# Kernel tuning notes

Hardware: AMD Instinct MI355X
Metric: run time of the kernel (lower is better)

## Reference

```python
import jax, jax.numpy as jnp
import numpy as np

V = 17  # number of skeleton joints (hard-coded in the torch module)
NUM_SUBSET = 3

def _dam_mask():
    # Reproduces the Python masking loops: zero block [12:17,12:17] and rows/cols {3,6,7,9,10}
    m = np.ones((V, V), np.float32)
    m[12:17, 12:17] = 0.0
    for j in (3, 6, 7, 9, 10):
        m[j, :] = 0.0
        m[:, j] = 0.0
    return jnp.asarray(m)

def setup_inputs() -> dict:
    key = jax.random.key(0)
    ks = jax.random.split(key, 8)
    N, Cin, Cout, T, G = 64, 64, 64, 256, 8
    return {
        "x": jax.random.normal(ks[0], (N, Cin, T, V), jnp.float32),
        "A_base": jax.random.uniform(ks[1], (NUM_SUBSET, V, V), jnp.float32),  # fixed adjacency buffer
        "DA": 0.01 * jax.random.normal(ks[2], (NUM_SUBSET, G, V, V), jnp.float32),   # DecoupleA param
        "DAM": 0.01 * jax.random.normal(ks[3], (NUM_SUBSET, G, V, V), jnp.float32),  # DecoupleAM param (masked, detached)
        "conv_w": jax.random.normal(ks[4], (NUM_SUBSET * Cout, Cin), jnp.float32) * (2.0 / Cin) ** 0.5,  # 1x1 conv
        "conv_b": jnp.zeros((NUM_SUBSET * Cout,), jnp.float32),
        "se_w": jax.random.normal(ks[5], (3,), jnp.float32) * 0.5,  # conv2_1: Conv1d(1,1,k=3,pad=1,no bias)
        "bn_gamma": jnp.full((Cout,), 1e-6, jnp.float32),  # bn_init(bn, 1e-6)
        "bn_beta": jnp.zeros((Cout,), jnp.float32),
    }

def reference(x, A_base, DA, DAM, conv_w, conv_b, se_w, bn_gamma, bn_beta):
    G = DA.shape[1]
    Cout = bn_gamma.shape[0]
    N, Cin, T, _ = x.shape
    # --- adjacency assembly: A (buffer, broadcast over groups) + DecoupleA + masked DecoupleAM ---
    A = A_base[:, None] + DA + DAM * _dam_mask()              # [3, G, V, V]
    # torch .repeat(1, out//groups, 1, 1) tiles along channel axis; + 0.04 from A_final loop
    A_final = jnp.tile(A, (1, Cout // G, 1, 1)) + 0.04        # [3, Cout, V, V]
    # --- 1x1 conv C_in -> 3*C_out ---
    m = jnp.einsum('nctv,kc->nktv', x, conv_w) + conv_b[None, :, None, None]
    m = m.reshape(N, NUM_SUBSET, Cout, T, V)
    # --- grouped adjacency aggregation (A_final has no batch dependence) ---
    m = jnp.einsum('nkctv,kcvw->nctw', m, A_final)            # [N, Cout, T, V]
    # --- SE-style channel attention: global avg pool -> Conv1d(k=3) over channels -> sigmoid gate ---
    p = m.mean(axis=(2, 3))                                   # [N, Cout]
    pp = jnp.pad(p, ((0, 0), (1, 1)))
    g = se_w[0] * pp[:, :-2] + se_w[1] * pp[:, 1:-1] + se_w[2] * pp[:, 2:]
    q = m + m * jax.nn.sigmoid(g)[:, :, None, None]
    # --- BatchNorm2d (training mode: batch stats over N,T,V) ---
    mu = q.mean(axis=(0, 2, 3), keepdims=True)
    var = q.var(axis=(0, 2, 3), keepdims=True)
    q = bn_gamma[None, :, None, None] * (q - mu) * jax.lax.rsqrt(var + 1e-5) + bn_beta[None, :, None, None]
    # --- residual (down == identity since in_channels == out_channels) and ReLU ---
    return jax.nn.relu(q + x)
```

## Files before the change

kernel.cpp:

```cpp
#include <hip/hip_runtime.h>
#include <math.h>

#define NN 64
#define CIN 64
#define COUT 64
#define TT 256
#define VV 17
#define NSUB 3
#define GG 8

#define WS_MB 0
#define WS_WBF 12288
#define WS_PSUM 18432
#define WS_SSQ 22528
#define WS_ACOEF 0
#define WS_BCOEF 4096
#define M2BF_BYTE_OFF 131072ull
#define M2BF_NEED (M2BF_BYTE_OFF + 2ull * 64 * 64 * 256 * 17)

typedef short bh8 __attribute__((ext_vector_type(8)));
typedef float f32x4 __attribute__((ext_vector_type(4)));
typedef float f32x16 __attribute__((ext_vector_type(16)));
typedef unsigned short u16t;

__device__ __forceinline__ unsigned bf16r(float f) {
    unsigned u = __builtin_bit_cast(unsigned, f);
    return (u + 0x7fffu + ((u >> 16) & 1u)) >> 16;
}
__device__ __forceinline__ float bf2f(unsigned us) {
    return __builtin_bit_cast(float, us << 16);
}

__device__ __forceinline__ float mfull(const float* Ab, const float* DA, const float* DAM,
                                       int s, int g, int v, int w) {
    const unsigned bad = (1u << 3) | (1u << 6) | (1u << 7) | (1u << 9) | (1u << 10);
    float mask = ((v >= 12 && w >= 12) || ((bad >> v) & 1) || ((bad >> w) & 1)) ? 0.f : 1.f;
    int src = ((s * GG + g) * VV + v) * VV + w;
    return Ab[(s * VV + v) * VV + w] + DA[src] + DAM[src] * mask + 0.04f;
}

__global__ void gcn_prep(const float* __restrict__ Ab, const float* __restrict__ DA,
                         const float* __restrict__ DAM, const float* __restrict__ convw,
                         float* __restrict__ ws) {
    int t0 = blockIdx.x * 256 + threadIdx.x;
    int stride = gridDim.x * 256;
    u16t* wbf = (u16t*)(ws + WS_WBF);
    for (int i = t0; i < 192 * 64; i += stride) wbf[i] = (u16t)bf16r(convw[i]);
    u16t* mb = (u16t*)(ws + WS_MB);
    for (int i = t0; i < NSUB * GG * 32 * 32; i += stride) {
        int k = i & 31, w = (i >> 5) & 31, g = (i >> 10) & 7, s = i >> 13;
        u16t val = 0;
        if (w < VV && k < VV) val = (u16t)bf16r(mfull(Ab, DA, DAM, s, g, k, w));
        mb[i] = val;
    }
}

template <int BFOUT>
__global__ __launch_bounds__(512, 4) void gcn_pass1(const float* __restrict__ x,
                                                    const float* __restrict__ convb,
                                                    const float* __restrict__ ws,
                                                    float* __restrict__ out,
                                                    u16t* __restrict__ m2b) {
    __shared__ __align__(16) unsigned char smem[73984];
    u16t* xsT = (u16t*)smem;
    u16t* Wl = (u16t*)(smem + 20736);
    u16t* mt = (u16t*)(smem + 48384);

    const int tid = threadIdx.x;
    const int wv = tid >> 6;
    const int l = tid & 63;
    const int c16 = l & 15;
    const int q4 = (l >> 4) & 3;
    const int c32 = l & 31;
    const int hi = l >> 5;
    const int n = blockIdx.x >> 3;

    {
        const unsigned* wsrc = (const unsigned*)(ws + WS_WBF);
        unsigned* wd = (unsigned*)Wl;
        for (int j = tid; j < 192 * 32; j += 512) wd[(j >> 5) * 36 + (j & 31)] = wsrc[j];
        unsigned* mz = (unsigned*)mt;
        for (int j = tid; j < 6400; j += 512) mz[j] = 0u;
    }

    const u16t* mb16 = (const u16t*)(ws + WS_MB);
    const int madj = (wv * 32 + c32) * 32;

    for (int k4 = 0; k4 < 4; ++k4) {
        const int tt = (blockIdx.x & 7) * 4 + k4;

        const float* xb = x + (size_t)n * 278528 + tt * 136;
        for (int task = tid; task < 1088; task += 512) {
            int oct = task / 136;
            int col = task - 136 * oct;
            const float* src = xb + (8 * oct) * 4352 + col;
            uint4 pk;
            pk.x = bf16r(src[0]) | (bf16r(src[4352]) << 16);
            pk.y = bf16r(src[2 * 4352]) | (bf16r(src[3 * 4352]) << 16);
            pk.z = bf16r(src[4 * 4352]) | (bf16r(src[5 * 4352]) << 16);
            pk.w = bf16r(src[6 * 4352]) | (bf16r(src[7 * 4352]) << 16);
            *(uint4*)&((unsigned*)xsT)[col * 36 + oct * 4] = pk;
        }
        __syncthreads();

        f32x16 D2[2];
        D2[0] = 0; D2[1] = 0;

        const int colm = 16 * wv + c16;
        const int tm = (colm * 241) >> 12;
        const int offm = tm * 24 + (colm - 17 * tm);

#pragma unroll
        for (int s = 0; s < 3; ++s) {
            bh8 Bc0 = *(const bh8*)&xsT[colm * 72 + 8 * q4];
            bh8 Bc1 = *(const bh8*)&xsT[colm * 72 + 32 + 8 * q4];
            f32x4 Dc0 = *(const f32x4*)(convb + s * 64 + 4 * q4);
            f32x4 Dc1 = *(const f32x4*)(convb + s * 64 + 16 + 4 * q4);
            {
                bh8 A;
                A = *(const bh8*)&Wl[(s * 64 + c16) * 72 + 8 * q4];
                Dc0 = __builtin_amdgcn_mfma_f32_16x16x32_bf16(A, Bc0, Dc0, 0, 0, 0);
                A = *(const bh8*)&Wl[(s * 64 + c16) * 72 + 32 + 8 * q4];
                Dc0 = __builtin_amdgcn_mfma_f32_16x16x32_bf16(A, Bc1, Dc0, 0, 0, 0);
                A = *(const bh8*)&Wl[(s * 64 + 16 + c16) * 72 + 8 * q4];
                Dc1 = __builtin_amdgcn_mfma_f32_16x16x32_bf16(A, Bc0, Dc1, 0, 0, 0);
                A = *(const bh8*)&Wl[(s * 64 + 16 + c16) * 72 + 32 + 8 * q4];
                Dc1 = __builtin_amdgcn_mfma_f32_16x16x32_bf16(A, Bc1, Dc1, 0, 0, 0);
            }

            if (s > 0) __syncthreads();
#pragma unroll
            for (int i = 0; i < 4; ++i) {
                mt[(4 * q4 + i) * 200 + offm] = (u16t)bf16r(Dc0[i]);
                mt[(16 + 4 * q4 + i) * 200 + offm] = (u16t)bf16r(Dc1[i]);
            }

            Dc0 = *(const f32x4*)(convb + s * 64 + 32 + 4 * q4);
            Dc1 = *(const f32x4*)(convb + s * 64 + 48 + 4 * q4);
            {
                bh8 A;
                A = *(const bh8*)&Wl[(s * 64 + 32 + c16) * 72 + 8 * q4];
                Dc0 = __builtin_amdgcn_mfma_f32_16x16x32_bf16(A, Bc0, Dc0, 0, 0, 0);
                A = *(const bh8*)&Wl[(s * 64 + 32 + c16) * 72 + 32 + 8 * q4];
                Dc0 = __builtin_amdgcn_mfma_f32_16x16x32_bf16(A, Bc1, Dc0, 0, 0, 0);
                A = *(const bh8*)&Wl[(s * 64 + 48 + c16) * 72 + 8 * q4];
                Dc1 = __builtin_amdgcn_mfma_f32_16x16x32_bf16(A, Bc0, Dc1, 0, 0, 0);
                A = *(const bh8*)&Wl[(s * 64 + 48 + c16) * 72 + 32 + 8 * q4];
                Dc1 = __builtin_amdgcn_mfma_f32_16x16x32_bf16(A, Bc1, Dc1, 0, 0, 0);
            }
#pragma unroll
            for (int i = 0; i < 4; ++i) {
                mt[(32 + 4 * q4 + i) * 200 + offm] = (u16t)bf16r(Dc0[i]);
                mt[(48 + 4 * q4 + i) * 200 + offm] = (u16t)bf16r(Dc1[i]);
            }

            if (wv < 4) {
                f32x4 Dc8 = *(const f32x4*)(convb + s * 64 + 16 * wv + 4 * q4);
                bh8 B80 = *(const bh8*)&xsT[(128 + c16) * 72 + 8 * q4];
                bh8 B81 = *(const bh8*)&xsT[(128 + c16) * 72 + 32 + 8 * q4];
                bh8 A0 = *(const bh8*)&Wl[(s * 64 + 16 * wv + c16) * 72 + 8 * q4];
                bh8 A1 = *(const bh8*)&Wl[(s * 64 + 16 * wv + c16) * 72 + 32 + 8 * q4];
                Dc8 = __builtin_amdgcn_mfma_f32_16x16x32_bf16(A0, B80, Dc8, 0, 0, 0);
                Dc8 = __builtin_amdgcn_mfma_f32_16x16x32_bf16(A1, B81, Dc8, 0, 0, 0);
                if (c16 < 8) {
                    int off8 = 7 * 24 + (9 + c16);
                    int co0 = 16 * wv + 4 * q4;
#pragma unroll
                    for (int i = 0; i < 4; ++i)
                        mt[(co0 + i) * 200 + off8] = (u16t)bf16r(Dc8[i]);
                }
            }

            bh8 Bs = *(const bh8*)&mb16[s * 8192 + madj + 8 * hi];
            u16t mv16 = mb16[s * 8192 + madj + 16];
            __syncthreads();

            bh8 b2 = {0, 0, 0, 0, 0, 0, 0, 0};
            b2[0] = hi ? (short)0 : (short)mv16;

#pragma unroll
            for (int p = 0; p < 2; ++p) {
                int co = wv + 8 * ((c32 >> 3) + 4 * p);
                int base = co * 200 + (c32 & 7) * 24 + 8 * hi;
                bh8 a0 = *(const bh8*)&mt[base];
                bh8 a1 = *(const bh8*)&mt[base + 16];
                D2[p] = __builtin_amdgcn_mfma_f32_32x32x16_bf16(a0, Bs, D2[p], 0, 0, 0);
                D2[p] = __builtin_amdgcn_mfma_f32_32x32x16_bf16(a1, b2, D2[p], 0, 0, 0);
            }
        }

        u16t* stg = xsT;
#pragma unroll
        for (int p = 0; p < 2; ++p)
#pragma unroll
            for (int reg = 0; reg < 16; ++reg) {
                const int cosel = reg >> 2;
                const int t = (reg & 3) + 4 * hi;
                const int co = wv + 8 * (cosel + 4 * p);
                if (c32 < 17) stg[co * 144 + t * 17 + c32] = (u16t)bf16r(D2[p][reg]);
            }
        __syncthreads();

        if (BFOUT) {
            u16t* gm = m2b + (size_t)(n * 32 + tt) * 8704;
#pragma unroll
            for (int it = 0; it < 3; ++it) {
                int c = tid + 512 * it;
                if (c < 1088) {
                    int co = c / 17, j = c - 17 * co;
                    *(uint4*)(gm + 8 * c) = *(const uint4*)&stg[co * 144 + 8 * j];
                }
            }
        } else {
            float* ob = out + (size_t)n * 278528 + tt * 136;
#pragma unroll
            for (int it = 0; it < 5; ++it) {
                int c = tid + 512 * it;
                if (c < 2176) {
                    int co = c / 34;
                    int pos = c - 34 * co;
                    uint2 u = *(const uint2*)&stg[co * 144 + pos * 4];
                    float4 v;
                    v.x = bf2f(u.x & 0xffffu);
                    v.y = bf2f(u.x >> 16);
                    v.z = bf2f(u.y & 0xffffu);
                    v.w = bf2f(u.y >> 16);
                    *(float4*)(ob + co * 4352 + pos * 4) = v;
                }
            }
        }
        __syncthreads();
    }
}

__device__ __forceinline__ void block_reduce2(float& s1, float& s2, float* r1, float* r2,
                                              int tid) {
#pragma unroll
    for (int m = 1; m < 64; m <<= 1) {
        s1 += __shfl_xor(s1, m);
        s2 += __shfl_xor(s2, m);
    }
    int wv = tid >> 6;
    if ((tid & 63) == 0) { r1[wv] = s1; r2[wv] = s2; }
    __syncthreads();
    if (tid == 0) {
        s1 = r1[0] + r1[1] + r1[2] + r1[3];
        s2 = r2[0] + r2[1] + r2[2] + r2[3];
    }
}

__global__ __launch_bounds__(256) void gcn_colsum_bf(const u16t* __restrict__ m2b,
                                                     float* __restrict__ psum,
                                                     float* __restrict__ ssq) {
    const int n = blockIdx.x >> 6, co = blockIdx.x & 63;
    const int tid = threadIdx.x;
    __shared__ float r1[4], r2[4];
    float s1 = 0.f, s2 = 0.f;
    for (int slot = tid; slot < 544; slot += 256) {
        int tt = slot / 17, i = slot - 17 * tt;
        const u16t* p = m2b + (size_t)(n * 32 + tt) * 8704 + co * 136 + i * 8;
        uint4 u = *(const uint4*)p;
#pragma unroll
        for (int k = 0; k < 4; ++k) {
            unsigned w = (&u.x)[k];
            float a = bf2f(w & 0xffffu), b = bf2f(w >> 16);
            s1 += a + b;
            s2 += a * a + b * b;
        }
    }
    block_reduce2(s1, s2, r1, r2, tid);
    if (tid == 0) {
        psum[n * 64 + co] = s1;
        ssq[n * 64 + co] = s2;
    }
}

__global__ __launch_bounds__(256) void gcn_colsum_f32(const float* __restrict__ m2,
                                                      float* __restrict__ psum,
                                                      float* __restrict__ ssq) {
    const int n = blockIdx.x >> 6, co = blockIdx.x & 63;
    const int tid = threadIdx.x;
    __shared__ float r1[4], r2[4];
    float s1 = 0.f, s2 = 0.f;
    const float4* p = (const float4*)(m2 + (size_t)n * 278528 + co * 4352);
    for (int u = tid; u < 1088; u += 256) {
        float4 v = p[u];
        s1 += v.x + v.y + v.z + v.w;
        s2 += v.x * v.x + v.y * v.y + v.z * v.z + v.w * v.w;
    }
    block_reduce2(s1, s2, r1, r2, tid);
    if (tid == 0) {
        psum[n * 64 + co] = s1;
        ssq[n * 64 + co] = s2;
    }
}

__global__ void gcn_stats(const float* __restrict__ se_w, const float* __restrict__ gamma,
                          const float* __restrict__ beta, float* __restrict__ ws) {
    __shared__ float ps[4096], sc[4096], q2s[4096];
    __shared__ float mu_s[64], inv_s[64];
    int tid = threadIdx.x;
    const float* psum = ws + WS_PSUM;
    const float* ssq = ws + WS_SSQ;
    float* acoef = ws + WS_ACOEF;
    float* bcoef = ws + WS_BCOEF;
    for (int i = tid; i < 4096; i += 256) ps[i] = psum[i] * (1.f / (TT * VV));
    __syncthreads();
    float w0 = se_w[0], w1 = se_w[1], w2 = se_w[2];
    for (int i = tid; i < 4096; i += 256) {
        int c = i & 63;
        float pm = (c > 0) ? ps[i - 1] : 0.f;
        float pp = (c < 63) ? ps[i + 1] : 0.f;
        float gg = w0 * pm + w1 * ps[i] + w2 * pp;
        float s = 1.f + 1.f / (1.f + expf(-gg));
        sc[i] = s;
        q2s[i] = s * s * ssq[i];
    }
    __syncthreads();
    if (tid < 64) {
        float mu = 0.f, e2 = 0.f;
        for (int nn = 0; nn < 64; ++nn) {
            mu += sc[nn * 64 + tid] * ps[nn * 64 + tid];
            e2 += q2s[nn * 64 + tid];
        }
        mu *= (1.f / 64.f);
        e2 *= (1.f / (64.f * TT * VV));
        float var = e2 - mu * mu;
        mu_s[tid] = mu;
        inv_s[tid] = rsqrtf(var + 1e-5f);
    }
    __syncthreads();
    for (int i = tid; i < 4096; i += 256) {
        int c = i & 63;
        float gin = gamma[c] * inv_s[c];
        acoef[i] = gin * sc[i];
        bcoef[i] = beta[c] - gin * mu_s[c];
    }
}

__global__ __launch_bounds__(256) void gcn_final_f32(const float* __restrict__ x,
                                                     const float* __restrict__ ws,
                                                     float* __restrict__ out) {
    const float* acoef = ws + WS_ACOEF;
    const float* bcoef = ws + WS_BCOEF;
    int i = blockIdx.x * 256 + threadIdx.x;
    const int total4 = (NN * COUT * TT * VV) / 4;
    if (i >= total4) return;
    int nc = i / ((TT * VV) / 4);
    float a = acoef[nc], b = bcoef[nc];
    float4 m = ((const float4*)out)[i];
    float4 xx = ((const float4*)x)[i];
    float4 r;
    r.x = fmaxf(fmaf(a, m.x, b) + xx.x, 0.f);
    r.y = fmaxf(fmaf(a, m.y, b) + xx.y, 0.f);
    r.z = fmaxf(fmaf(a, m.z, b) + xx.z, 0.f);
    r.w = fmaxf(fmaf(a, m.w, b) + xx.w, 0.f);
    ((float4*)out)[i] = r;
}

__global__ __launch_bounds__(256) void gcn_final_bf16(const float* __restrict__ x,
                                                      const float* __restrict__ ws,
                                                      const u16t* __restrict__ m2b,
                                                      float* __restrict__ out) {
    const float* acoef = ws + WS_ACOEF;
    const float* bcoef = ws + WS_BCOEF;
    const int bt = blockIdx.x;
    const int n = bt >> 5, tt = bt & 31;
    const u16t* gm = m2b + (size_t)bt * 8704;
    const size_t base = (size_t)n * 278528 + tt * 136;
    const int tid = threadIdx.x;
#pragma unroll
    for (int it = 0; it < 5; ++it) {
        int task = tid + 256 * it;
        if (task < 1088) {
            int co = task / 17, j = task - 17 * co;
            float a = acoef[n * 64 + co], b = bcoef[n * 64 + co];
            uint4 u = *(const uint4*)(gm + 8 * task);
            const float* xp = x + base + co * 4352 + 8 * j;
            float4 x0 = *(const float4*)xp;
            float4 x1 = *(const float4*)(xp + 4);
            float4 r0, r1;
            r0.x = fmaxf(fmaf(a, bf2f(u.x & 0xffffu), b) + x0.x, 0.f);
            r0.y = fmaxf(fmaf(a, bf2f(u.x >> 16), b) + x0.y, 0.f);
            r0.z = fmaxf(fmaf(a, bf2f(u.y & 0xffffu), b) + x0.z, 0.f);
            r0.w = fmaxf(fmaf(a, bf2f(u.y >> 16), b) + x0.w, 0.f);
            r1.x = fmaxf(fmaf(a, bf2f(u.z & 0xffffu), b) + x1.x, 0.f);
            r1.y = fmaxf(fmaf(a, bf2f(u.z >> 16), b) + x1.y, 0.f);
            r1.z = fmaxf(fmaf(a, bf2f(u.w & 0xffffu), b) + x1.z, 0.f);
            r1.w = fmaxf(fmaf(a, bf2f(u.w >> 16), b) + x1.w, 0.f);
            float* op = out + base + co * 4352 + 8 * j;
            *(float4*)op = r0;
            *(float4*)(op + 4) = r1;
        }
    }
}

extern "C" void kernel_launch(void* const* d_in, const int* in_sizes, int n_in,
                              void* d_out, int out_size, void* d_ws, size_t ws_size,
                              hipStream_t stream) {
    const float* x = (const float*)d_in[0];
    const float* Ab = (const float*)d_in[1];
    const float* DA = (const float*)d_in[2];
    const float* DAM = (const float*)d_in[3];
    const float* convw = (const float*)d_in[4];
    const float* convb = (const float*)d_in[5];
    const float* sew = (const float*)d_in[6];
    const float* gamma = (const float*)d_in[7];
    const float* beta = (const float*)d_in[8];
    float* out = (float*)d_out;
    float* ws = (float*)d_ws;
    u16t* m2b = (u16t*)((char*)d_ws + M2BF_BYTE_OFF);
    const bool bfpath = ws_size >= M2BF_NEED;

    gcn_prep<<<16, 256, 0, stream>>>(Ab, DA, DAM, convw, ws);
    if (bfpath) {
        gcn_pass1<1><<<512, 512, 0, stream>>>(x, convb, ws, out, m2b);
        gcn_colsum_bf<<<4096, 256, 0, stream>>>(m2b, ws + WS_PSUM, ws + WS_SSQ);
        gcn_stats<<<1, 256, 0, stream>>>(sew, gamma, beta, ws);
        gcn_final_bf16<<<2048, 256, 0, stream>>>(x, ws, m2b, out);
    } else {
        gcn_pass1<0><<<512, 512, 0, stream>>>(x, convb, ws, out, m2b);
        gcn_colsum_f32<<<4096, 256, 0, stream>>>(out, ws + WS_PSUM, ws + WS_SSQ);
        gcn_stats<<<1, 256, 0, stream>>>(sew, gamma, beta, ws);
        const int total4 = (NN * COUT * TT * VV) / 4;
        gcn_final_f32<<<(total4 + 255) / 256, 256, 0, stream>>>(x, ws, out);
    }
}
```

Measured before the change: 109.7 us.

## Fuse per-channel sum/sumsq into pass1 and prefetch next x tile into registers

Removes the separate colsum kernel by computing per-(n,channel) sum and sum of squares inside gcn_pass1. It reduces them with wave shuffles and LDS atomics, then issues global atomics into psum/ssq, which gcn_prep now zeroes. It also software-pipelines the x load: the next time tile is read into registers during the last subset iteration, hiding global load latency. The stats now come from fp32 accumulators before bf16 rounding, and the float atomics make the summation order nondeterministic. Register pressure rises under launch_bounds(512,4).

```diff
diff --git a/kernel.cpp b/kernel.cpp
--- a/kernel.cpp
+++ b/kernel.cpp
@@ -53,6 +53,7 @@
         if (w < VV && k < VV) val = (u16t)bf16r(mfull(Ab, DA, DAM, s, g, k, w));
         mb[i] = val;
     }
+    for (int i = t0; i < 8192; i += stride) ws[WS_PSUM + i] = 0.f;
 }
 
 template <int BFOUT>
@@ -60,11 +61,15 @@
                                                     const float* __restrict__ convb,
                                                     const float* __restrict__ ws,
                                                     float* __restrict__ out,
-                                                    u16t* __restrict__ m2b) {
-    __shared__ __align__(16) unsigned char smem[73984];
+                                                    u16t* __restrict__ m2b,
+                                                    float* __restrict__ psum,
+                                                    float* __restrict__ ssq) {
+    __shared__ __align__(16) unsigned char smem[74496];
     u16t* xsT = (u16t*)smem;
     u16t* Wl = (u16t*)(smem + 20736);
     u16t* mt = (u16t*)(smem + 48384);
+    float* psL = (float*)(smem + 73984);
+    float* sqL = (float*)(smem + 74240);
 
     const int tid = threadIdx.x;
     const int wv = tid >> 6;
@@ -75,12 +80,26 @@
     const int hi = l >> 5;
     const int n = blockIdx.x >> 3;
 
+    const int oct0 = tid / 136, col0 = tid - 136 * oct0;
+    const int t1i = tid + 512;
+    const int oct1 = t1i / 136, col1 = t1i - 136 * oct1;
+
+    float xr[16];
+    {
+        const float* xb0 = x + (size_t)n * 278528 + ((blockIdx.x & 7) * 4) * 136;
+        const float* s0 = xb0 + (8 * oct0) * 4352 + col0;
+        const float* s1 = xb0 + (8 * oct1) * 4352 + col1;
+#pragma unroll
+        for (int k = 0; k < 8; ++k) { xr[k] = s0[k * 4352]; xr[8 + k] = s1[k * 4352]; }
+    }
+
     {
         const unsigned* wsrc = (const unsigned*)(ws + WS_WBF);
         unsigned* wd = (unsigned*)Wl;
         for (int j = tid; j < 192 * 32; j += 512) wd[(j >> 5) * 36 + (j & 31)] = wsrc[j];
         unsigned* mz = (unsigned*)mt;
         for (int j = tid; j < 6400; j += 512) mz[j] = 0u;
+        if (tid < 64) { psL[tid] = 0.f; sqL[tid] = 0.f; }
     }
 
     const u16t* mb16 = (const u16t*)(ws + WS_MB);
@@ -89,17 +108,27 @@
     for (int k4 = 0; k4 < 4; ++k4) {
         const int tt = (blockIdx.x & 7) * 4 + k4;
 
-        const float* xb = x + (size_t)n * 278528 + tt * 136;
-        for (int task = tid; task < 1088; task += 512) {
-            int oct = task / 136;
-            int col = task - 136 * oct;
-            const float* src = xb + (8 * oct) * 4352 + col;
+        {
+            uint4 pk;
+            pk.x = bf16r(xr[0]) | (bf16r(xr[1]) << 16);
+            pk.y = bf16r(xr[2]) | (bf16r(xr[3]) << 16);
+            pk.z = bf16r(xr[4]) | (bf16r(xr[5]) << 16);
+            pk.w = bf16r(xr[6]) | (bf16r(xr[7]) << 16);
+            *(uint4*)&((unsigned*)xsT)[col0 * 36 + oct0 * 4] = pk;
+            pk.x = bf16r(xr[8]) | (bf16r(xr[9]) << 16);
+            pk.y = bf16r(xr[10]) | (bf16r(xr[11]) << 16);
+            pk.z = bf16r(xr[12]) | (bf16r(xr[13]) << 16);
+            pk.w = bf16r(xr[14]) | (bf16r(xr[15]) << 16);
+            *(uint4*)&((unsigned*)xsT)[col1 * 36 + oct1 * 4] = pk;
+        }
+        if (tid < 64) {
+            const float* src = x + (size_t)n * 278528 + tt * 136 + 56 * 4352 + (72 + tid);
             uint4 pk;
             pk.x = bf16r(src[0]) | (bf16r(src[4352]) << 16);
             pk.y = bf16r(src[2 * 4352]) | (bf16r(src[3 * 4352]) << 16);
             pk.z = bf16r(src[4 * 4352]) | (bf16r(src[5 * 4352]) << 16);
             pk.w = bf16r(src[6 * 4352]) | (bf16r(src[7 * 4352]) << 16);
-            *(uint4*)&((unsigned*)xsT)[col * 36 + oct * 4] = pk;
+            *(uint4*)&((unsigned*)xsT)[(72 + tid) * 36 + 28] = pk;
         }
         __syncthreads();
 
@@ -171,6 +200,14 @@
                 }
             }
 
+            if (s == 2 && k4 < 3) {
+                const float* xb1 = x + (size_t)n * 278528 + (tt + 1) * 136;
+                const float* s0 = xb1 + (8 * oct0) * 4352 + col0;
+                const float* s1p = xb1 + (8 * oct1) * 4352 + col1;
+#pragma unroll
+                for (int k = 0; k < 8; ++k) { xr[k] = s0[k * 4352]; xr[8 + k] = s1p[k * 4352]; }
+            }
+
             bh8 Bs = *(const bh8*)&mb16[s * 8192 + madj + 8 * hi];
             u16t mv16 = mb16[s * 8192 + madj + 16];
             __syncthreads();
@@ -198,6 +235,22 @@
                 const int t = (reg & 3) + 4 * hi;
                 const int co = wv + 8 * (cosel + 4 * p);
                 if (c32 < 17) stg[co * 144 + t * 17 + c32] = (u16t)bf16r(D2[p][reg]);
+            }
+#pragma unroll
+        for (int p = 0; p < 2; ++p)
+#pragma unroll
+            for (int cs = 0; cs < 4; ++cs) {
+                float v0 = D2[p][4 * cs], v1 = D2[p][4 * cs + 1];
+                float v2 = D2[p][4 * cs + 2], v3 = D2[p][4 * cs + 3];
+                float s1 = (v0 + v1) + (v2 + v3);
+                float s2 = fmaf(v0, v0, fmaf(v1, v1, fmaf(v2, v2, v3 * v3)));
+                s1 += __shfl_xor(s1, 1); s2 += __shfl_xor(s2, 1);
+                s1 += __shfl_xor(s1, 2); s2 += __shfl_xor(s2, 2);
+                s1 += __shfl_xor(s1, 4); s2 += __shfl_xor(s2, 4);
+                if ((l & 7) == 0) {
+                    atomicAdd(&psL[wv + 8 * (cs + 4 * p)], s1);
+                    atomicAdd(&sqL[wv + 8 * (cs + 4 * p)], s2);
+                }
             }
         __syncthreads();
 
@@ -231,67 +284,10 @@
         }
         __syncthreads();
     }
-}
-
-__device__ __forceinline__ void block_reduce2(float& s1, float& s2, float* r1, float* r2,
-                                              int tid) {
-#pragma unroll
-    for (int m = 1; m < 64; m <<= 1) {
-        s1 += __shfl_xor(s1, m);
-        s2 += __shfl_xor(s2, m);
-    }
-    int wv = tid >> 6;
-    if ((tid & 63) == 0) { r1[wv] = s1; r2[wv] = s2; }
-    __syncthreads();
-    if (tid == 0) {
-        s1 = r1[0] + r1[1] + r1[2] + r1[3];
-        s2 = r2[0] + r2[1] + r2[2] + r2[3];
-    }
-}
-
-__global__ __launch_bounds__(256) void gcn_colsum_bf(const u16t* __restrict__ m2b,
-                                                     float* __restrict__ psum,
-                                                     float* __restrict__ ssq) {
-    const int n = blockIdx.x >> 6, co = blockIdx.x & 63;
-    const int tid = threadIdx.x;
-    __shared__ float r1[4], r2[4];
-    float s1 = 0.f, s2 = 0.f;
-    for (int slot = tid; slot < 544; slot += 256) {
-        int tt = slot / 17, i = slot - 17 * tt;
-        const u16t* p = m2b + (size_t)(n * 32 + tt) * 8704 + co * 136 + i * 8;
-        uint4 u = *(const uint4*)p;
-#pragma unroll
-        for (int k = 0; k < 4; ++k) {
-            unsigned w = (&u.x)[k];
-            float a = bf2f(w & 0xffffu), b = bf2f(w >> 16);
-            s1 += a + b;
-            s2 += a * a + b * b;
-        }
-    }
-    block_reduce2(s1, s2, r1, r2, tid);
-    if (tid == 0) {
-        psum[n * 64 + co] = s1;
-        ssq[n * 64 + co] = s2;
-    }
-}
-
-__global__ __launch_bounds__(256) void gcn_colsum_f32(const float* __restrict__ m2,
-                                                      float* __restrict__ psum,
-                                                      float* __restrict__ ssq) {
-    const int n = blockIdx.x >> 6, co = blockIdx.x & 63;
-    const int tid = threadIdx.x;
-    __shared__ float r1[4], r2[4];
-    float s1 = 0.f, s2 = 0.f;
-    const float4* p = (const float4*)(m2 + (size_t)n * 278528 + co * 4352);
-    for (int u = tid; u < 1088; u += 256) {
-        float4 v = p[u];
-        s1 += v.x + v.y + v.z + v.w;
-        s2 += v.x * v.x + v.y * v.y + v.z * v.z + v.w * v.w;
-    }
-    block_reduce2(s1, s2, r1, r2, tid);
-    if (tid == 0) {
-        psum[n * 64 + co] = s1;
-        ssq[n * 64 + co] = s2;
+
+    if (tid < 64) {
+        atomicAdd(&psum[n * 64 + tid], psL[tid]);
+        atomicAdd(&ssq[n * 64 + tid], sqL[tid]);
     }
 }
 
@@ -414,13 +410,13 @@
 
     gcn_prep<<<16, 256, 0, stream>>>(Ab, DA, DAM, convw, ws);
     if (bfpath) {
-        gcn_pass1<1><<<512, 512, 0, stream>>>(x, convb, ws, out, m2b);
-        gcn_colsum_bf<<<4096, 256, 0, stream>>>(m2b, ws + WS_PSUM, ws + WS_SSQ);
+        gcn_pass1<1><<<512, 512, 0, stream>>>(x, convb, ws, out, m2b,
+                                              ws + WS_PSUM, ws + WS_SSQ);
         gcn_stats<<<1, 256, 0, stream>>>(sew, gamma, beta, ws);
         gcn_final_bf16<<<2048, 256, 0, stream>>>(x, ws, m2b, out);
     } else {
-        gcn_pass1<0><<<512, 512, 0, stream>>>(x, convb, ws, out, m2b);
-        gcn_colsum_f32<<<4096, 256, 0, stream>>>(out, ws + WS_PSUM, ws + WS_SSQ);
+        gcn_pass1<0><<<512, 512, 0, stream>>>(x, convb, ws, out, m2b,
+                                              ws + WS_PSUM, ws + WS_SSQ);
         gcn_stats<<<1, 256, 0, stream>>>(sew, gamma, beta, ws);
         const int total4 = (NN * COUT * TT * VV) / 4;
         gcn_final_f32<<<(total4 + 255) / 256, 256, 0, stream>>>(x, ws, out);
```

Measured after the change: 157.6 us. 43.6% more time.
